# Kernel tuning notes

Hardware: AMD Instinct MI355X
Metric: run time of the kernel (lower is better)

Reference implementation:

```python
import jax, jax.numpy as jnp
import numpy as np

S, B, C = 7, 2, 20
LC, LN = 5.0, 0.5  # lambda_coord, lambda_noobj
CELL = 1.0 / S


def _iou(b1, b2):
    # center (x, y, w, h) boxes, broadcastable [..., 4]
    x1a, y1a = b1[..., 0] - b1[..., 2] / 2, b1[..., 1] - b1[..., 3] / 2
    x2a, y2a = b1[..., 0] + b1[..., 2] / 2, b1[..., 1] + b1[..., 3] / 2
    x1b, y1b = b2[..., 0] - b2[..., 2] / 2, b2[..., 1] - b2[..., 3] / 2
    x2b, y2b = b2[..., 0] + b2[..., 2] / 2, b2[..., 1] + b2[..., 3] / 2
    iw = jnp.maximum(jnp.minimum(x2a, x2b) - jnp.maximum(x1a, x1b), 0.0)
    ih = jnp.maximum(jnp.minimum(y2a, y2b) - jnp.maximum(y1a, y1b), 0.0)
    inter = iw * ih
    union = b1[..., 2] * b1[..., 3] + b2[..., 2] * b2[..., 3] - inter
    return inter / jnp.maximum(union, 1e-10)


def setup_inputs() -> dict:
    key = jax.random.key(0)
    k1, k2, k3 = jax.random.split(key, 3)
    N, T = 16384, 16
    outputs = jax.random.normal(k1, (N, S, S, B * 5 + C), dtype=jnp.float32)
    # normalized xywh, kept strictly inside (0,1) so grid indices are valid
    boxes = jax.random.uniform(k2, (N, T, 4), dtype=jnp.float32, minval=0.01, maxval=0.99)
    labels = jax.random.randint(k3, (N, T), 1, C + 1)  # class labels in 1..C
    return {"outputs": outputs, "boxes": boxes, "labels": labels}


def reference(outputs, boxes, labels):
    N = outputs.shape[0]
    T = boxes.shape[1]
    bbox = outputs[..., : B * 5].reshape(N, S, S, B, 5)
    conf = bbox[..., 4]                         # [N,S,S,B]
    cls_logits = outputs[..., B * 5:]           # [N,S,S,C]
    # decode predicted centers to absolute image coords (as in the original)
    gx = jnp.arange(S, dtype=outputs.dtype)[None, :, None]  # column index
    gy = jnp.arange(S, dtype=outputs.dtype)[:, None, None]  # row index
    px = (bbox[..., 0] + gx) * CELL
    py = (bbox[..., 1] + gy) * CELL
    pred = jnp.stack([px, py, bbox[..., 2], bbox[..., 3]], axis=-1)  # [N,S,S,B,4]

    tx, ty, tw, th = boxes[..., 0], boxes[..., 1], boxes[..., 2], boxes[..., 3]  # [N,T]
    gxi = (tx * S).astype(jnp.int32)
    gyi = (ty * S).astype(jnp.int32)
    offx = tx * S - gxi.astype(tx.dtype)
    offy = ty * S - gyi.astype(ty.dtype)

    bi = jnp.arange(N)[:, None]  # [N,1] broadcasts with [N,T]
    cell_pred = pred[bi, gyi, gxi]          # [N,T,B,4]
    cell_conf = conf[bi, gyi, gxi]          # [N,T,B]
    cell_cls = cls_logits[bi, gyi, gxi]     # [N,T,C]

    ious = _iou(boxes[:, :, None, :], cell_pred)   # [N,T,B]
    best = (B - 1) - jnp.argmax(ious[..., ::-1], axis=-1)  # [N,T]

    bp = jnp.take_along_axis(cell_pred, best[:, :, None, None], axis=2)[:, :, 0, :]  # [N,T,4]
    bconf = jnp.take_along_axis(cell_conf, best[:, :, None], axis=2)[:, :, 0]        # [N,T]

    eps = 1e-6
    box_loss = (
        (bp[..., 0] - offx) ** 2
        + (bp[..., 1] - offy) ** 2
        + (jnp.sqrt(jnp.maximum(bp[..., 2], eps)) - jnp.sqrt(jnp.maximum(tw, eps))) ** 2
        + (jnp.sqrt(jnp.maximum(bp[..., 3], eps)) - jnp.sqrt(jnp.maximum(th, eps))) ** 2
    ).sum(axis=-1)                                     # [N]
    obj_loss = ((bconf - 1.0) ** 2).sum(axis=-1)        # [N]

    probs = jax.nn.softmax(cell_cls, axis=-1)           # [N,T,C]
    onehot = jax.nn.one_hot(labels - 1, C, dtype=probs.dtype)
    class_loss = ((probs - onehot) ** 2).sum(axis=-1).sum(axis=-1)  # [N]

    obj_mask = jnp.zeros((N, S, S, B), dtype=bool).at[bi, gyi, gxi, best].set(True)
    nm = ~obj_mask
    cnt = nm.sum(axis=(1, 2, 3)).astype(conf.dtype)     # always > 0 (T < S*S*B)
    noobj_loss = (conf ** 2 * nm).sum(axis=(1, 2, 3)) / cnt  # mean over unmasked conf

    per_img = LC * box_loss + class_loss + obj_loss + LN * noobj_loss
    return per_img.mean()
```

## Files before the change

kernel.cpp:

```cpp
#include <hip/hip_runtime.h>

#define NCH   30
#define NCONF 98
#define IMGF  1470
#define LCf 5.0f
#define LNf 0.5f

#define AS1 __attribute__((address_space(1)))
#define AS3 __attribute__((address_space(3)))

template<int CTRL>
__device__ __forceinline__ float dppf(float v) {
    return __int_as_float(__builtin_amdgcn_update_dpp(
        0, __float_as_int(v), CTRL, 0xF, 0xF, true));
}
#define QP_XOR1 0xB1
#define QP_XOR2 0x4E
#define QP_B0   0x00
#define ROW_ROR4 0x124
#define ROW_ROR8 0x128

__device__ __forceinline__ float rlane(float v, int k) {
    return __int_as_float(__builtin_amdgcn_readlane(__float_as_int(v), k));
}

__device__ __forceinline__ float img_partial(const float* __restrict__ img,
                                             float4 bx, int lab,
                                             volatile unsigned char* sm,
                                             int lane, int t, int q, float cf1)
{
    float ns = cf1 * cf1;
    if (lane < NCONF - 64) {
        int s2 = lane + 64;
        int c2 = s2 >> 1, b2 = s2 & 1;
        float cf2 = img[c2 * NCH + b2 * 5 + 4];
        ns += cf2 * cf2;
    }

    const float tx = bx.x, ty = bx.y, tw = bx.z, th = bx.w;
    const float fx = tx * 7.0f, fy = ty * 7.0f;
    const int gxi = (int)fx, gyi = (int)fy;
    const float offx = fx - (float)gxi;
    const float offy = fy - (float)gyi;
    const int cellIdx = gyi * 7 + gxi;
    const float* cell = img + cellIdx * NCH;

    float px = 0.f, py = 0.f, pw = 0.f, ph = 0.f, pc = 0.f, iou_own = 0.f;
    if (q < 2) {
        float rx = cell[q * 5 + 0];
        float ry = cell[q * 5 + 1];
        pw       = cell[q * 5 + 2];
        ph       = cell[q * 5 + 3];
        pc       = cell[q * 5 + 4];
        px = (rx + (float)gxi) * (1.0f / 7.0f);
        py = (ry + (float)gyi) * (1.0f / 7.0f);

        float x1a = tx - tw * 0.5f, y1a = ty - th * 0.5f;
        float x2a = tx + tw * 0.5f, y2a = ty + th * 0.5f;
        float x1b = px - pw * 0.5f, y1b = py - ph * 0.5f;
        float x2b = px + pw * 0.5f, y2b = py + ph * 0.5f;
        float iw = fmaxf(fminf(x2a, x2b) - fmaxf(x1a, x1b), 0.0f);
        float ih = fmaxf(fminf(y2a, y2b) - fmaxf(y1a, y1b), 0.0f);
        float inter = iw * ih;
        float uni = tw * th + pw * ph - inter;
        iou_own = inter / fmaxf(uni, 1e-10f);
    }
    const float iou_other = dppf<QP_XOR1>(iou_own);
    int bestq = 0;
    if (q < 2) {
        float i0 = (q == 0) ? iou_own   : iou_other;
        float i1 = (q == 0) ? iou_other : iou_own;
        bestq = (i1 >= i0) ? 1 : 0;
    }
    const int best = __builtin_amdgcn_update_dpp(0, bestq, QP_B0, 0xF, 0xF, true);
    const int s = cellIdx * 2 + best;

    float contrib = 0.0f;
    const float eps = 1e-6f;
    if (q == best) {
        float dx = px - offx, dy = py - offy;
        float dw = sqrtf(fmaxf(pw, eps)) - sqrtf(fmaxf(tw, eps));
        float dh = sqrtf(fmaxf(ph, eps)) - sqrtf(fmaxf(th, eps));
        float box_l = dx * dx + dy * dy + dw * dw + dh * dh;
        float obj_l = (pc - 1.0f) * (pc - 1.0f);
        contrib = LCf * box_l + obj_l;
    }

    if (q == best) sm[s] = (unsigned char)lane;
    asm volatile("s_waitcnt lgkmcnt(0)" ::: "memory");
    __builtin_amdgcn_sched_barrier(0);
    const bool winner = (q == best) && (sm[s] == (unsigned char)lane);
    const unsigned long long bal = __ballot(winner);
    const int mc = __popcll(bal);
    const float ms = winner ? pc * pc : 0.0f;

    {
        float cv[5];
        #pragma unroll
        for (int i = 0; i < 5; ++i) cv[i] = cell[10 + q * 5 + i];
        float m = fmaxf(fmaxf(fmaxf(cv[0], cv[1]), fmaxf(cv[2], cv[3])), cv[4]);
        m = fmaxf(m, dppf<QP_XOR1>(m));
        m = fmaxf(m, dppf<QP_XOR2>(m));
        float esum = 0.f, e2 = 0.f, elab = 0.f;
        #pragma unroll
        for (int i = 0; i < 5; ++i) {
            float e = __expf(cv[i] - m);
            esum += e; e2 += e * e;
            if (q * 5 + i == lab) elab = e;
        }
        esum += dppf<QP_XOR1>(esum);  esum += dppf<QP_XOR2>(esum);
        e2   += dppf<QP_XOR1>(e2);    e2   += dppf<QP_XOR2>(e2);
        elab += dppf<QP_XOR1>(elab);  elab += dppf<QP_XOR2>(elab);
        if (q == 0) {
            float inv = 1.0f / esum;
            contrib += e2 * inv * inv - 2.0f * elab * inv + 1.0f;
        }
    }

    const float invDen = 1.0f / (98.0f - (float)mc);
    return contrib + LNf * (ns - ms) * invDen;
}

__global__ __launch_bounds__(128) void yolo_loss_kernel(
    const float* __restrict__ outputs,
    const float* __restrict__ boxes,
    const int*   __restrict__ labels,
    float*       __restrict__ per_img)
{
    const int tid  = threadIdx.x;
    const int wave = tid >> 6;
    const int lane = tid & 63;
    const int t    = lane >> 2;
    const int q    = lane & 3;
    const int n    = blockIdx.x * 2 + wave;

    __shared__ __align__(16) float s_img[2 * IMGF];
    __shared__ unsigned char       s_m[2][112];

    const float4 bx = reinterpret_cast<const float4*>(boxes)[(size_t)n * 16 + t];
    const int   lab = labels[(size_t)n * 16 + t] - 1;

    const float* gsrc = outputs + (size_t)n * IMGF;
    char* wbase = (char*)&s_img[wave * IMGF];
    const int odd = wave & 1;
    {
        const float* sgp = odd ? gsrc : (gsrc + IMGF - 2);
        char*        slp = odd ? wbase : (wbase + (size_t)(IMGF - 2) * 4);
        if (lane < 2) {
            __builtin_amdgcn_global_load_lds((const AS1 void*)(sgp + lane),
                                             (AS3 void*)slp, 4, 0, 0);
        }
        const float4* g4 = reinterpret_cast<const float4*>(gsrc + (odd ? 2 : 0));
        char* l4 = wbase + (odd ? 8 : 0);
        #pragma unroll
        for (int k = 0; k < 5; ++k) {
            __builtin_amdgcn_global_load_lds(
                (const AS1 void*)(g4 + k * 64 + lane),
                (AS3 void*)(l4 + (size_t)k * 1024), 16, 0, 0);
        }
        if (lane < 367 - 320) {
            __builtin_amdgcn_global_load_lds(
                (const AS1 void*)(g4 + 320 + lane),
                (AS3 void*)(l4 + (size_t)5 * 1024), 16, 0, 0);
        }
    }

    const float* img = &s_img[wave * IMGF];

    asm volatile("s_waitcnt vmcnt(2)" ::: "memory");
    __builtin_amdgcn_sched_barrier(0);
    const float cf1 = img[(lane >> 1) * NCH + (lane & 1) * 5 + 4];

    asm volatile("s_waitcnt vmcnt(0)" ::: "memory");
    __builtin_amdgcn_sched_barrier(0);

    float v = img_partial(img, bx, lab, s_m[wave], lane, t, q, cf1);

    v += dppf<QP_XOR1>(v);
    v += dppf<QP_XOR2>(v);
    v += dppf<ROW_ROR4>(v);
    v += dppf<ROW_ROR8>(v);
    const float tot = (rlane(v, 0) + rlane(v, 16)) + (rlane(v, 32) + rlane(v, 48));
    if (lane == 0) per_img[n] = tot;
}

__global__ __launch_bounds__(1024) void reduce_mean_kernel(
    const float* __restrict__ per_img, float* __restrict__ out, int N)
{
    __shared__ double sd[16];
    double acc = 0.0;
    const float4* p4 = reinterpret_cast<const float4*>(per_img);
    for (int i = threadIdx.x; i < N / 4; i += 1024) {
        float4 v = p4[i];
        acc += (double)v.x + (double)v.y + (double)v.z + (double)v.w;
    }
    #pragma unroll
    for (int off = 32; off > 0; off >>= 1) acc += __shfl_xor(acc, off);
    if ((threadIdx.x & 63) == 0) sd[threadIdx.x >> 6] = acc;
    __syncthreads();
    if (threadIdx.x == 0) {
        double tsum = 0.0;
        #pragma unroll
        for (int w = 0; w < 16; ++w) tsum += sd[w];
        out[0] = (float)(tsum / (double)N);
    }
}

extern "C" void kernel_launch(void* const* d_in, const int* in_sizes, int n_in,
                              void* d_out, int out_size, void* d_ws, size_t ws_size,
                              hipStream_t stream) {
    const float* outputs = (const float*)d_in[0];
    const float* boxes   = (const float*)d_in[1];
    const int*   labels  = (const int*)d_in[2];
    float* out = (float*)d_out;

    const int N  = in_sizes[0] / IMGF;
    const int nb = N / 2;
    float* per_img = (float*)d_ws;

    yolo_loss_kernel<<<nb, 128, 0, stream>>>(outputs, boxes, labels, per_img);
    reduce_mean_kernel<<<1, 1024, 0, stream>>>(per_img, out, N);
}
```

Baseline: 24.37 us.

## Replace per-image store and reduce kernel with striped atomics; simplify aligned LDS load

Each wave now atomically adds its image loss into one of 64 padded accumulator slots instead of writing per-image results. The 1024-thread reduction kernel is replaced by a tiny 64-lane finalize kernel, plus a memset of the accumulators. The image load is changed to use only aligned 16-byte loads from a rounded-down base, with an offset pointer into LDS, which drops the odd/even special-case scalar loads. This adds a memset launch and float atomics, whose summation order is nondeterministic, and the reduction now accumulates in float rather than double.

```diff
diff --git a/kernel.cpp b/kernel.cpp
--- a/kernel.cpp
+++ b/kernel.cpp
@@ -3,6 +3,9 @@
 #define NCH   30
 #define NCONF 98
 #define IMGF  1470
+#define IMG4  368
+#define NACC  64
+#define ASTR  16
 #define LCf 5.0f
 #define LNf 0.5f
 
@@ -125,7 +128,7 @@
     const float* __restrict__ outputs,
     const float* __restrict__ boxes,
     const int*   __restrict__ labels,
-    float*       __restrict__ per_img)
+    float*       __restrict__ acc)
 {
     const int tid  = threadIdx.x;
     const int wave = tid >> 6;
@@ -134,38 +137,28 @@
     const int q    = lane & 3;
     const int n    = blockIdx.x * 2 + wave;
 
-    __shared__ __align__(16) float s_img[2 * IMGF];
+    __shared__ __align__(16) float s_img[2 * IMG4 * 4];
     __shared__ unsigned char       s_m[2][112];
 
     const float4 bx = reinterpret_cast<const float4*>(boxes)[(size_t)n * 16 + t];
     const int   lab = labels[(size_t)n * 16 + t] - 1;
 
     const float* gsrc = outputs + (size_t)n * IMGF;
-    char* wbase = (char*)&s_img[wave * IMGF];
-    const int odd = wave & 1;
-    {
-        const float* sgp = odd ? gsrc : (gsrc + IMGF - 2);
-        char*        slp = odd ? wbase : (wbase + (size_t)(IMGF - 2) * 4);
-        if (lane < 2) {
-            __builtin_amdgcn_global_load_lds((const AS1 void*)(sgp + lane),
-                                             (AS3 void*)slp, 4, 0, 0);
-        }
-        const float4* g4 = reinterpret_cast<const float4*>(gsrc + (odd ? 2 : 0));
-        char* l4 = wbase + (odd ? 8 : 0);
-        #pragma unroll
-        for (int k = 0; k < 5; ++k) {
-            __builtin_amdgcn_global_load_lds(
-                (const AS1 void*)(g4 + k * 64 + lane),
-                (AS3 void*)(l4 + (size_t)k * 1024), 16, 0, 0);
-        }
-        if (lane < 367 - 320) {
-            __builtin_amdgcn_global_load_lds(
-                (const AS1 void*)(g4 + 320 + lane),
-                (AS3 void*)(l4 + (size_t)5 * 1024), 16, 0, 0);
-        }
-    }
-
-    const float* img = &s_img[wave * IMGF];
+    const uintptr_t gb = (uintptr_t)gsrc & ~(uintptr_t)15;
+    const float4* g4 = reinterpret_cast<const float4*>(gb);
+    char* wb = (char*)&s_img[wave * (IMG4 * 4)];
+    #pragma unroll
+    for (int k = 0; k < 5; ++k) {
+        __builtin_amdgcn_global_load_lds(
+            (const AS1 void*)(g4 + k * 64 + lane),
+            (AS3 void*)(wb + (size_t)k * 1024), 16, 0, 0);
+    }
+    if (lane < IMG4 - 320) {
+        __builtin_amdgcn_global_load_lds(
+            (const AS1 void*)(g4 + 320 + lane),
+            (AS3 void*)(wb + (size_t)5 * 1024), 16, 0, 0);
+    }
+    const float* img = (const float*)(wb + ((uintptr_t)gsrc - gb));
 
     asm volatile("s_waitcnt vmcnt(2)" ::: "memory");
     __builtin_amdgcn_sched_barrier(0);
@@ -181,29 +174,20 @@
     v += dppf<ROW_ROR4>(v);
     v += dppf<ROW_ROR8>(v);
     const float tot = (rlane(v, 0) + rlane(v, 16)) + (rlane(v, 32) + rlane(v, 48));
-    if (lane == 0) per_img[n] = tot;
-}
-
-__global__ __launch_bounds__(1024) void reduce_mean_kernel(
-    const float* __restrict__ per_img, float* __restrict__ out, int N)
+    if (lane == 0) atomicAdd(&acc[(n & (NACC - 1)) * ASTR], tot);
+}
+
+__global__ __launch_bounds__(64) void finalize_kernel(
+    const float* __restrict__ acc, float* __restrict__ out, float invN)
 {
-    __shared__ double sd[16];
-    double acc = 0.0;
-    const float4* p4 = reinterpret_cast<const float4*>(per_img);
-    for (int i = threadIdx.x; i < N / 4; i += 1024) {
-        float4 v = p4[i];
-        acc += (double)v.x + (double)v.y + (double)v.z + (double)v.w;
-    }
-    #pragma unroll
-    for (int off = 32; off > 0; off >>= 1) acc += __shfl_xor(acc, off);
-    if ((threadIdx.x & 63) == 0) sd[threadIdx.x >> 6] = acc;
-    __syncthreads();
-    if (threadIdx.x == 0) {
-        double tsum = 0.0;
-        #pragma unroll
-        for (int w = 0; w < 16; ++w) tsum += sd[w];
-        out[0] = (float)(tsum / (double)N);
-    }
+    const int lane = threadIdx.x;
+    float v = acc[lane * ASTR];
+    v += dppf<QP_XOR1>(v);
+    v += dppf<QP_XOR2>(v);
+    v += dppf<ROW_ROR4>(v);
+    v += dppf<ROW_ROR8>(v);
+    const float tot = (rlane(v, 0) + rlane(v, 16)) + (rlane(v, 32) + rlane(v, 48));
+    if (lane == 0) out[0] = tot * invN;
 }
 
 extern "C" void kernel_launch(void* const* d_in, const int* in_sizes, int n_in,
@@ -214,10 +198,10 @@
     const int*   labels  = (const int*)d_in[2];
     float* out = (float*)d_out;
 
-    const int N  = in_sizes[0] / IMGF;
-    const int nb = N / 2;
-    float* per_img = (float*)d_ws;
-
-    yolo_loss_kernel<<<nb, 128, 0, stream>>>(outputs, boxes, labels, per_img);
-    reduce_mean_kernel<<<1, 1024, 0, stream>>>(per_img, out, N);
-}
+    const int N = in_sizes[0] / IMGF;
+    float* acc = (float*)d_ws;
+
+    hipMemsetAsync(acc, 0, NACC * ASTR * sizeof(float), stream);
+    yolo_loss_kernel<<<N / 2, 128, 0, stream>>>(outputs, boxes, labels, acc);
+    finalize_kernel<<<1, 64, 0, stream>>>(acc, out, 1.0f / (float)N);
+}
```

New measurement: 28.30 us. 16.1% more time.
